# Optimization experiments

Measured on AMD Instinct MI355X. Metric: run time of the kernel, lower is better.

The kernel has to match this reference:

```python
import jax, jax.numpy as jnp
import numpy as np
from jax import lax

STRIDE = 1
PAD = 1


def conv2d(x, w, b, stride=STRIDE, pad=PAD):
    out = lax.conv_general_dilated(x, w, (stride, stride), [(pad, pad), (pad, pad)],
                                   dimension_numbers=('NCHW', 'OIHW', 'NCHW'))
    return out + b[None, :, None, None]


def bilinear_gather(x, py, px):
    # x: [B,C,H,W]; py,px: [B,K,Ho,Wo] float sample coords. Zero outside.
    B, C, H, W = x.shape
    y0 = jnp.floor(py)
    x0 = jnp.floor(px)
    wy = (py - y0)[:, None]  # [B,1,K,Ho,Wo]
    wx = (px - x0)[:, None]
    y0i = y0.astype(jnp.int32)
    x0i = x0.astype(jnp.int32)
    xf = x.reshape(B, C, H * W)

    def gather(yi, xi):
        valid = ((yi >= 0) & (yi < H) & (xi >= 0) & (xi < W))
        yc = jnp.clip(yi, 0, H - 1)
        xc = jnp.clip(xi, 0, W - 1)
        idx = (yc * W + xc).reshape(B, 1, -1)
        v = jnp.take_along_axis(xf, idx, axis=2).reshape(B, C, *yi.shape[1:])
        return v * valid[:, None].astype(x.dtype)

    v00 = gather(y0i, x0i)
    v01 = gather(y0i, x0i + 1)
    v10 = gather(y0i + 1, x0i)
    v11 = gather(y0i + 1, x0i + 1)
    return (v00 * (1 - wy) * (1 - wx) + v01 * (1 - wy) * wx
            + v10 * wy * (1 - wx) + v11 * wy * wx)  # [B,C,K,Ho,Wo]


def deform_conv2d(x, offset, weight, bias, mask_mod, stride=STRIDE, pad=PAD):
    # torchvision.ops.deform_conv2d semantics, groups=1, dilation=1.
    B, C, H, W = x.shape
    Co, Ci, Kh, Kw = weight.shape
    K = Kh * Kw
    Ho, Wo = offset.shape[2], offset.shape[3]
    off = offset.reshape(B, K, 2, Ho, Wo)
    dy, dx = off[:, :, 0], off[:, :, 1]
    ky, kx = jnp.meshgrid(jnp.arange(Kh), jnp.arange(Kw), indexing='ij')
    base_y = (jnp.arange(Ho) * stride - pad).astype(x.dtype)
    base_x = (jnp.arange(Wo) * stride - pad).astype(x.dtype)
    py = dy + ky.reshape(K)[None, :, None, None] + base_y[None, None, :, None]
    px = dx + kx.reshape(K)[None, :, None, None] + base_x[None, None, None, :]
    vals = bilinear_gather(x, py, px)  # [B,C,K,Ho,Wo]
    if mask_mod is not None:
        vals = vals * mask_mod[:, None]  # modulation mask [B,K,Ho,Wo]
    out = jnp.einsum('bckhw,ock->bohw', vals, weight.reshape(Co, Ci, K))
    if bias is not None:
        out = out + bias[None, :, None, None]
    return out


def setup_inputs() -> dict:
    key = jax.random.key(0)
    ks = jax.random.split(key, 8)
    B, Cin, Cout, H, W, Kh, Kw = 4, 64, 64, 128, 128, 3, 3
    K = Kh * Kw
    n = Cin * Kh * Kw
    stdv = 1.0 / np.sqrt(n)
    inp = jax.random.normal(ks[0], (B, Cin, H, W), dtype=jnp.float32)
    mask_in = (jax.random.uniform(ks[1], (B, 1, H, W)) > 0.25).astype(jnp.float32)
    weight = jax.random.uniform(ks[2], (Cout, Cin, Kh, Kw), minval=-stdv, maxval=stdv, dtype=jnp.float32)
    bias = jnp.zeros((Cout,), jnp.float32)
    offset_w = jax.random.normal(ks[3], (2 * K, Cin + 1, Kh, Kw), dtype=jnp.float32) * 0.01
    offset_b = jnp.zeros((2 * K,), jnp.float32)
    mask_w = jax.random.normal(ks[4], (K, Cin + 1, Kh, Kw), dtype=jnp.float32) * 0.01
    mask_b = jnp.zeros((K,), jnp.float32)
    return {'input': inp, 'mask_in': mask_in, 'weight': weight, 'bias': bias,
            'offset_w': offset_w, 'offset_b': offset_b, 'mask_w': mask_w, 'mask_b': mask_b}


def reference(input, mask_in, weight, bias, offset_w, offset_b, mask_w, mask_b):
    xm = jnp.concatenate([input, mask_in], axis=1)
    offset = conv2d(xm, offset_w, offset_b)
    C = input.shape[1]
    Kh, Kw = weight.shape[2], weight.shape[3]
    slide_winsize = float(C * Kh * Kw)  # 1*C*Kh*Kw (maskUpdater out-channels = 1)
    # Partial-conv mask propagation (torch.no_grad in original)
    mask_rep = jnp.broadcast_to(mask_in, input.shape)
    ones_w = jnp.ones((1, C, Kh, Kw), input.dtype)
    um = lax.stop_gradient(deform_conv2d(mask_rep, offset, ones_w, None, None))  # [B,1,Ho,Wo]
    update_mask = jnp.clip(um, 0.0, 1.0)
    dcn_mask = jax.nn.sigmoid(conv2d(xm, mask_w, mask_b))
    raw_out = deform_conv2d(input, offset, weight, bias, dcn_mask)
    output = raw_out * update_mask
    return output, update_mask
```

## Files before the change

### kernel.cpp

```cpp
#include <hip/hip_runtime.h>

#define HH 128
#define WW 128
#define HWSZ (HH*WW)
#define NB 4
#define KK 9
#define PS (HWSZ*8)
#define IMS (12*PS)

typedef _Float16 half8 __attribute__((ext_vector_type(8)));
typedef _Float16 h2    __attribute__((ext_vector_type(2)));
typedef float f32x4    __attribute__((ext_vector_type(4)));

union U4 { uint4 v; unsigned a[4]; };
union HU { unsigned u; h2 h; };

__device__ __forceinline__ short f2h(float f) {
    union { _Float16 h; short s; } u; u.h = (_Float16)f; return u.s;
}
__device__ __forceinline__ void gl_lds16(const short* g, short* l) {
    __builtin_amdgcn_global_load_lds(
        (const __attribute__((address_space(1))) void*)g,
        (__attribute__((address_space(3))) void*)l, 16, 0, 0);
}
__device__ __forceinline__ void gl_lds4(const float* g, float* l) {
    __builtin_amdgcn_global_load_lds(
        (const __attribute__((address_space(1))) void*)g,
        (__attribute__((address_space(3))) void*)l, 4, 0, 0);
}

__global__ __launch_bounds__(256) void prep_kernel(
    const float* __restrict__ input,
    const float* __restrict__ mask_in,
    const float* __restrict__ weight,
    const float* __restrict__ offset_w,
    const float* __restrict__ mask_w,
    short* __restrict__ xt2,
    short* __restrict__ wd2,
    short* __restrict__ wc2)
{
    __shared__ short lds[64 * 104];
    int bid = blockIdx.x;
    if (bid < 1024) {
        int wg = ((bid & 7) << 7) | (bid >> 3);
        int g0 = wg * 64;
        int b  = g0 >> 14;
        int p0 = g0 & (HWSZ - 1);
        int px = threadIdx.x & 63;
        int cq = threadIdx.x >> 6;
#pragma unroll
        for (int it = 0; it < 24; ++it) {
            int c = it * 4 + cq;
            float v;
            if (c < 64)       v = input[((size_t)(b * 64 + c)) * HWSZ + p0 + px];
            else if (c == 64) v = mask_in[(size_t)b * HWSZ + p0 + px];
            else              v = 0.f;
            lds[px * 104 + c] = f2h(v);
        }
        __syncthreads();
#pragma unroll
        for (int it = 0; it < 3; ++it) {
            int idx = it * 256 + threadIdx.x;
            if (idx < 768) {
                int ppx = idx / 12, cb = idx - ppx * 12;
                uint4 v = *(const uint4*)&lds[ppx * 104 + cb * 8];
                *(uint4*)&xt2[(size_t)b * IMS + (size_t)cb * PS + (size_t)(p0 + ppx) * 8] = v;
            }
        }
    } else {
        int idx = (bid - 1024) * 256 + threadIdx.x;
        if (idx < 36864) {
            int j = idx & 7, l = (idx >> 3) & 63, f = idx >> 9;
            int nt = f & 3, t9 = f >> 2;
            int k = t9 % 9, ks = t9 / 9;
            int o = nt * 16 + (l & 15);
            int c = ks * 32 + ((l >> 4) & 3) * 8 + j;
            wd2[idx] = f2h(weight[(o * 64 + c) * 9 + k]);
        }
        if (idx < 27648) {
            int j = idx & 7, l = (idx >> 3) & 63, f = idx >> 9;
            int nt = f & 1, t9 = f >> 1;
            int k = t9 % 9, ks = t9 / 9;
            int o = nt * 16 + (l & 15);
            int c = ks * 32 + ((l >> 4) & 3) * 8 + j;
            float v = 0.f;
            if (c <= 64) {
                if (o < 18)      v = offset_w[(o * 65 + c) * 9 + k];
                else if (o < 27) v = mask_w[((o - 18) * 65 + c) * 9 + k];
            }
            wc2[idx] = f2h(v);
        }
    }
}

__global__ __launch_bounds__(256, 3) void fused_conv_deform(
    const short* __restrict__ xt2, const float* __restrict__ mask_in,
    const half8* __restrict__ wc, const half8* __restrict__ wd,
    const float* __restrict__ offset_b, const float* __restrict__ mask_b,
    const float* __restrict__ bias,
    float* __restrict__ out, float* __restrict__ upd)
{
    __shared__ short xsm[8 * 5 * 68 * 8];
    __shared__ float msm[5 * 68];
    __shared__ float offsm[64 * 28];

    int bid = blockIdx.x;
    int wg = ((bid & 7) << 7) | (bid >> 3);
    int wid = threadIdx.x >> 6, lane = threadIdx.x & 63;
    int r = lane & 15, lg = lane >> 4;
    int gblk = wg * 64;
    int b = gblk >> 14;
    int pblk = gblk & (HWSZ - 1);
    int ib = pblk >> 7, j0b = pblk & 127;
    int g0 = gblk + wid * 16;
    int gp = g0 + r;
    int p = gp & (HWSZ - 1);
    int i = p >> 7, j = p & 127;
    const short* xq = xt2 + (size_t)b * IMS + (size_t)lg * PS;
    const float* mb = mask_in + (size_t)b * HWSZ;

    {
        const short* xg = xt2 + (size_t)b * IMS;
#pragma unroll
        for (int it = 0; it < 11; ++it) {
            int idx = it * 256 + threadIdx.x;
            if (idx < 2720) {
                int rb = idx / 68, tc = idx - rb * 68;
                int cb = rb / 5,  tr = rb - cb * 5;
                int row_g = min(max(ib - 2 + tr, 0), HH - 1);
                int col_g = min(max(j0b - 2 + tc, 0), WW - 1);
                gl_lds16(&xg[(size_t)cb * PS + (size_t)(row_g * WW + col_g) * 8],
                         &xsm[idx * 8]);
            }
        }
#pragma unroll
        for (int it = 0; it < 2; ++it) {
            int idx = it * 256 + threadIdx.x;
            if (idx < 340) {
                int tr = idx / 68, tc = idx - tr * 68;
                int row_g = min(max(ib - 2 + tr, 0), HH - 1);
                int col_g = min(max(j0b - 2 + tc, 0), WW - 1);
                gl_lds4(&mb[row_g * WW + col_g], &msm[idx]);
            }
        }
    }

    {
        f32x4 ca0 = {0,0,0,0}, ca1 = {0,0,0,0};
#pragma unroll
        for (int t = 0; t < 9; ++t) {
            int yy = i + t / 3 - 1, xx = j + t % 3 - 1;
            bool v = ((unsigned)yy < HH) && ((unsigned)xx < WW);
            int nb = (v ? yy * WW + xx : 0) * 8;
            union { half8 s8; uint4 u; } A[3];
#pragma unroll
            for (int ks = 0; ks < 3; ++ks) {
                A[ks].u = *(const uint4*)(xq + (size_t)ks * 4 * PS + nb);
                if (!v) { A[ks].u.x = 0; A[ks].u.y = 0; A[ks].u.z = 0; A[ks].u.w = 0; }
            }
#pragma unroll
            for (int ks = 0; ks < 3; ++ks) {
                const half8* wck = wc + ((ks * 9 + t) * 2) * 64 + lane;
                half8 B0 = wck[0];
                half8 B1 = wck[64];
                ca0 = __builtin_amdgcn_mfma_f32_16x16x32_f16(A[ks].s8, B0, ca0, 0, 0, 0);
                ca1 = __builtin_amdgcn_mfma_f32_16x16x32_f16(A[ks].s8, B1, ca1, 0, 0, 0);
            }
        }
        int oc = lane & 15, pr0 = lg * 4;
#pragma unroll
        for (int rr = 0; rr < 4; ++rr) {
            int pxl = wid * 16 + pr0 + rr;
            offsm[pxl * 28 + oc] = ca0[rr] + offset_b[oc];
            int oc2 = 16 + oc;
            if (oc2 < 18) {
                offsm[pxl * 28 + oc2] = ca1[rr] + offset_b[oc2];
            } else if (oc2 < 27) {
                float z = ca1[rr] + mask_b[oc2 - 18];
                offsm[pxl * 28 + oc2] = 1.f / (1.f + __expf(-z));
            }
        }
    }
    asm volatile("s_waitcnt vmcnt(0)" ::: "memory");
    __syncthreads();

    float ov[28];
    {
        int pxl = wid * 16 + r;
#pragma unroll
        for (int q = 0; q < 7; ++q) {
            float4 t = *(const float4*)&offsm[pxl * 28 + q * 4];
            ov[4*q+0] = t.x; ov[4*q+1] = t.y; ov[4*q+2] = t.z; ov[4*q+3] = t.w;
        }
    }

    f32x4 acc0 = {0,0,0,0}, acc1 = {0,0,0,0}, acc2 = {0,0,0,0}, acc3 = {0,0,0,0};
    float um = 0.f;

#pragma unroll
    for (int k = 0; k < KK; ++k) {
        float dy = ov[2*k], dx = ov[2*k+1], m = ov[18+k];
        float py  = dy + (float)(k / 3 + i - 1);
        float pxx = dx + (float)(k % 3 + j - 1);
        float fy = floorf(py), fx = floorf(pxx);
        float wy = py - fy, wx = pxx - fx;
        int y0 = (int)fy, x0 = (int)fx;
        int y1 = y0 + 1, x1 = x0 + 1;
        bool vy0 = (unsigned)y0 < HH, vy1 = (unsigned)y1 < HH;
        bool vx0 = (unsigned)x0 < WW, vx1 = (unsigned)x1 < WW;
        int yc0 = min(max(y0, 0), HH - 1), yc1 = min(max(y1, 0), HH - 1);
        int xc0 = min(max(x0, 0), WW - 1), xc1 = min(max(x1, 0), WW - 1);
        float r00 = (vy0 && vx0) ? (1.f - wy) * (1.f - wx) : 0.f;
        float r01 = (vy0 && vx1) ? (1.f - wy) * wx : 0.f;
        float r10 = (vy1 && vx0) ? wy * (1.f - wx) : 0.f;
        float r11 = (vy1 && vx1) ? wy * wx : 0.f;

        int tr0 = yc0 - ib + 2, tr1 = yc1 - ib + 2;
        int tc0 = xc0 - j0b + 2, tc1 = xc1 - j0b + 2;
        bool in00 = ((unsigned)tr0 < 5u) & ((unsigned)tc0 < 68u);
        bool in01 = ((unsigned)tr0 < 5u) & ((unsigned)tc1 < 68u);
        bool in10 = ((unsigned)tr1 < 5u) & ((unsigned)tc0 < 68u);
        bool in11 = ((unsigned)tr1 < 5u) & ((unsigned)tc1 < 68u);
        int trc0 = min(max(tr0, 0), 4), trc1 = min(max(tr1, 0), 4);
        int tcc0 = min(max(tc0, 0), 67), tcc1 = min(max(tc1, 0), 67);
        int l00 = (trc0 * 68 + tcc0), l01 = (trc0 * 68 + tcc1);
        int l10 = (trc1 * 68 + tcc0), l11 = (trc1 * 68 + tcc1);

        U4 g00[2], g01[2], g10[2], g11[2];
#pragma unroll
        for (int ks = 0; ks < 2; ++ks) {
            const short* xs = xsm + (size_t)(ks * 4 + lg) * (5 * 68 * 8);
            g00[ks].v = *(const uint4*)(xs + l00 * 8);
            g01[ks].v = *(const uint4*)(xs + l01 * 8);
            g10[ks].v = *(const uint4*)(xs + l10 * 8);
            g11[ks].v = *(const uint4*)(xs + l11 * 8);
        }
        float m00 = msm[l00], m01 = msm[l01], m10 = msm[l10], m11 = msm[l11];

        if (!__all(in00 & in01 & in10 & in11)) {
            int p00 = yc0 * WW + xc0, p01 = yc0 * WW + xc1;
            int p10 = yc1 * WW + xc0, p11 = yc1 * WW + xc1;
            if (!in00) {
                g00[0].v = *(const uint4*)(xq + (size_t)p00 * 8);
                g00[1].v = *(const uint4*)(xq + 4 * PS + (size_t)p00 * 8);
                m00 = mb[p00];
            }
            if (!in01) {
                g01[0].v = *(const uint4*)(xq + (size_t)p01 * 8);
                g01[1].v = *(const uint4*)(xq + 4 * PS + (size_t)p01 * 8);
                m01 = mb[p01];
            }
            if (!in10) {
                g10[0].v = *(const uint4*)(xq + (size_t)p10 * 8);
                g10[1].v = *(const uint4*)(xq + 4 * PS + (size_t)p10 * 8);
                m10 = mb[p10];
            }
            if (!in11) {
                g11[0].v = *(const uint4*)(xq + (size_t)p11 * 8);
                g11[1].v = *(const uint4*)(xq + 4 * PS + (size_t)p11 * 8);
                m11 = mb[p11];
            }
        }

        um += r00 * m00 + r01 * m01 + r10 * m10 + r11 * m11;

        float w00 = r00 * m, w01 = r01 * m, w10 = r10 * m, w11 = r11 * m;
        h2 w00h = { (_Float16)w00, (_Float16)w00 };
        h2 w01h = { (_Float16)w01, (_Float16)w01 };
        h2 w10h = { (_Float16)w10, (_Float16)w10 };
        h2 w11h = { (_Float16)w11, (_Float16)w11 };

#pragma unroll
        for (int ks = 0; ks < 2; ++ks) {
            union { half8 s8; unsigned u[4]; } A;
#pragma unroll
            for (int q = 0; q < 4; ++q) {
                HU a00, a01, a10, a11, res;
                a00.u = g00[ks].a[q]; a01.u = g01[ks].a[q];
                a10.u = g10[ks].a[q]; a11.u = g11[ks].a[q];
                h2 acc = a00.h * w00h;
                acc = a01.h * w01h + acc;
                acc = a10.h * w10h + acc;
                acc = a11.h * w11h + acc;
                res.h = acc;
                A.u[q] = res.u;
            }
            const half8* wbk = wd + ((ks * 9 + k) * 4) * 64 + lane;
            half8 B0 = wbk[0];
            half8 B1 = wbk[64];
            half8 B2 = wbk[128];
            half8 B3 = wbk[192];
            acc0 = __builtin_amdgcn_mfma_f32_16x16x32_f16(A.s8, B0, acc0, 0, 0, 0);
            acc1 = __builtin_amdgcn_mfma_f32_16x16x32_f16(A.s8, B1, acc1, 0, 0, 0);
            acc2 = __builtin_amdgcn_mfma_f32_16x16x32_f16(A.s8, B2, acc2, 0, 0, 0);
            acc3 = __builtin_amdgcn_mfma_f32_16x16x32_f16(A.s8, B3, acc3, 0, 0, 0);
        }
    }

    um = fminf(fmaxf(64.f * um, 0.f), 1.f);
    if (lane < 16) upd[g0 + lane] = um;

    int oc = lane & 15;
    int pr0 = lg * 4;
    float u[4];
#pragma unroll
    for (int rr = 0; rr < 4; ++rr) u[rr] = __shfl(um, pr0 + rr, 64);

    __syncthreads();
    float* outsm = (float*)xsm;
#define STORE_NT(ACC, NT)                                                     \
    {                                                                         \
        float bo = bias[(NT) * 16 + oc];                                      \
        _Pragma("unroll")                                                     \
        for (int rr = 0; rr < 4; ++rr) {                                      \
            int pxl = wid * 16 + pr0 + rr;                                    \
            outsm[pxl * 65 + (NT) * 16 + oc] = (ACC[rr] + bo) * u[rr];        \
        }                                                                     \
    }
    STORE_NT(acc0, 0)
    STORE_NT(acc1, 1)
    STORE_NT(acc2, 2)
    STORE_NT(acc3, 3)
#undef STORE_NT
    __syncthreads();
    {
        int ch = threadIdx.x >> 2, q = threadIdx.x & 3;
        float tmp[16];
#pragma unroll
        for (int mI = 0; mI < 16; ++mI)
            tmp[mI] = outsm[(q * 16 + mI) * 65 + ch];
        float4* dst = (float4*)(out + ((size_t)(b * 64 + ch)) * HWSZ + pblk + q * 16);
#pragma unroll
        for (int gq = 0; gq < 4; ++gq) {
            float4 v = { tmp[4*gq], tmp[4*gq+1], tmp[4*gq+2], tmp[4*gq+3] };
            dst[gq] = v;
        }
    }
}

extern "C" void kernel_launch(void* const* d_in, const int* in_sizes, int n_in,
                              void* d_out, int out_size, void* d_ws, size_t ws_size,
                              hipStream_t stream) {
    const float* input    = (const float*)d_in[0];
    const float* mask_in  = (const float*)d_in[1];
    const float* weight   = (const float*)d_in[2];
    const float* bias     = (const float*)d_in[3];
    const float* offset_w = (const float*)d_in[4];
    const float* offset_b = (const float*)d_in[5];
    const float* mask_w   = (const float*)d_in[6];
    const float* mask_b   = (const float*)d_in[7];

    float* out = (float*)d_out;
    float* upd = out + (size_t)NB * 64 * HWSZ;

    short* wd2 = (short*)d_ws;
    short* wc2 = wd2 + 36864;
    short* xt2 = wc2 + 27648;

    hipLaunchKernelGGL(prep_kernel, dim3(1168), dim3(256), 0, stream,
                       input, mask_in, weight, offset_w, mask_w, xt2, wd2, wc2);
    hipLaunchKernelGGL(fused_conv_deform, dim3(1024), dim3(256), 0, stream,
                       xt2, mask_in, (const half8*)wc2, (const half8*)wd2,
                       offset_b, mask_b, bias, out, upd);
}
```

Measured before the change: 43.17 us.

## Process two output rows per block and feed offset conv from the LDS tile

Each workgroup now covers a 2x64 pixel tile instead of 64 pixels, staging a 6-row halo tile in LDS. The offset/mask conv reads its A operands from that LDS tile (and folds the mask channel in via msm) rather than from global memory. Weight fragments are loaded once and reused across both rows. Offsets are stored as fp16 in LDS. The grid halves and launch bounds drop to 2 blocks per CU, which raises per-thread register use and lowers occupancy; the fp16 offsets reduce precision of the sampling coordinates.

```diff
diff --git a/kernel.cpp b/kernel.cpp
--- a/kernel.cpp
+++ b/kernel.cpp
@@ -7,6 +7,9 @@
 #define KK 9
 #define PS (HWSZ*8)
 #define IMS (12*PS)
+#define TROWS 6
+#define TCOLS 68
+#define TPX (TROWS*TCOLS)
 
 typedef _Float16 half8 __attribute__((ext_vector_type(8)));
 typedef _Float16 h2    __attribute__((ext_vector_type(2)));
@@ -93,247 +96,318 @@
     }
 }
 
-__global__ __launch_bounds__(256, 3) void fused_conv_deform(
+__global__ __launch_bounds__(256, 2) void fused_conv_deform(
     const short* __restrict__ xt2, const float* __restrict__ mask_in,
     const half8* __restrict__ wc, const half8* __restrict__ wd,
     const float* __restrict__ offset_b, const float* __restrict__ mask_b,
     const float* __restrict__ bias,
     float* __restrict__ out, float* __restrict__ upd)
 {
-    __shared__ short xsm[8 * 5 * 68 * 8];
-    __shared__ float msm[5 * 68];
-    __shared__ float offsm[64 * 28];
+    __shared__ short xsm[8 * TPX * 8];
+    __shared__ float msm[TPX];
+    __shared__ short offsm[128 * 32];
 
     int bid = blockIdx.x;
-    int wg = ((bid & 7) << 7) | (bid >> 3);
-    int wid = threadIdx.x >> 6, lane = threadIdx.x & 63;
+    int wg = ((bid & 7) << 6) | (bid >> 3);
+    int w = threadIdx.x >> 6, lane = threadIdx.x & 63;
     int r = lane & 15, lg = lane >> 4;
-    int gblk = wg * 64;
-    int b = gblk >> 14;
-    int pblk = gblk & (HWSZ - 1);
-    int ib = pblk >> 7, j0b = pblk & 127;
-    int g0 = gblk + wid * 16;
-    int gp = g0 + r;
-    int p = gp & (HWSZ - 1);
-    int i = p >> 7, j = p & 127;
-    const short* xq = xt2 + (size_t)b * IMS + (size_t)lg * PS;
+    int b = wg >> 7;
+    int rem = wg & 127;
+    int ib = (rem >> 1) * 2;
+    int j0b = (rem & 1) * 64;
+    int jw = j0b + w * 16;
+    int jj0 = jw + r;
+
+    const short* xg = xt2 + (size_t)b * IMS;
+    const short* xq = xg + (size_t)lg * PS;
     const float* mb = mask_in + (size_t)b * HWSZ;
 
-    {
-        const short* xg = xt2 + (size_t)b * IMS;
-#pragma unroll
-        for (int it = 0; it < 11; ++it) {
-            int idx = it * 256 + threadIdx.x;
-            if (idx < 2720) {
-                int rb = idx / 68, tc = idx - rb * 68;
-                int cb = rb / 5,  tr = rb - cb * 5;
-                int row_g = min(max(ib - 2 + tr, 0), HH - 1);
-                int col_g = min(max(j0b - 2 + tc, 0), WW - 1);
-                gl_lds16(&xg[(size_t)cb * PS + (size_t)(row_g * WW + col_g) * 8],
-                         &xsm[idx * 8]);
-            }
-        }
+#pragma unroll
+    for (int cb = 0; cb < 8; ++cb) {
 #pragma unroll
         for (int it = 0; it < 2; ++it) {
             int idx = it * 256 + threadIdx.x;
-            if (idx < 340) {
-                int tr = idx / 68, tc = idx - tr * 68;
-                int row_g = min(max(ib - 2 + tr, 0), HH - 1);
-                int col_g = min(max(j0b - 2 + tc, 0), WW - 1);
-                gl_lds4(&mb[row_g * WW + col_g], &msm[idx]);
-            }
-        }
-    }
-
-    {
-        f32x4 ca0 = {0,0,0,0}, ca1 = {0,0,0,0};
-#pragma unroll
-        for (int t = 0; t < 9; ++t) {
-            int yy = i + t / 3 - 1, xx = j + t % 3 - 1;
-            bool v = ((unsigned)yy < HH) && ((unsigned)xx < WW);
-            int nb = (v ? yy * WW + xx : 0) * 8;
-            union { half8 s8; uint4 u; } A[3];
-#pragma unroll
-            for (int ks = 0; ks < 3; ++ks) {
-                A[ks].u = *(const uint4*)(xq + (size_t)ks * 4 * PS + nb);
-                if (!v) { A[ks].u.x = 0; A[ks].u.y = 0; A[ks].u.z = 0; A[ks].u.w = 0; }
-            }
-#pragma unroll
-            for (int ks = 0; ks < 3; ++ks) {
-                const half8* wck = wc + ((ks * 9 + t) * 2) * 64 + lane;
-                half8 B0 = wck[0];
-                half8 B1 = wck[64];
-                ca0 = __builtin_amdgcn_mfma_f32_16x16x32_f16(A[ks].s8, B0, ca0, 0, 0, 0);
-                ca1 = __builtin_amdgcn_mfma_f32_16x16x32_f16(A[ks].s8, B1, ca1, 0, 0, 0);
-            }
-        }
-        int oc = lane & 15, pr0 = lg * 4;
-#pragma unroll
-        for (int rr = 0; rr < 4; ++rr) {
-            int pxl = wid * 16 + pr0 + rr;
-            offsm[pxl * 28 + oc] = ca0[rr] + offset_b[oc];
-            int oc2 = 16 + oc;
-            if (oc2 < 18) {
-                offsm[pxl * 28 + oc2] = ca1[rr] + offset_b[oc2];
-            } else if (oc2 < 27) {
-                float z = ca1[rr] + mask_b[oc2 - 18];
-                offsm[pxl * 28 + oc2] = 1.f / (1.f + __expf(-z));
-            }
+            if (idx < TPX) {
+                int tr = idx / TCOLS, tc = idx - tr * TCOLS;
+                int rg = min(max(ib - 2 + tr, 0), HH - 1);
+                int cg = min(max(j0b - 2 + tc, 0), WW - 1);
+                gl_lds16(&xg[(size_t)cb * PS + (size_t)(rg * WW + cg) * 8],
+                         &xsm[(cb * TPX + idx) * 8]);
+            }
+        }
+    }
+#pragma unroll
+    for (int it = 0; it < 2; ++it) {
+        int idx = it * 256 + threadIdx.x;
+        if (idx < TPX) {
+            int tr = idx / TCOLS, tc = idx - tr * TCOLS;
+            int rg = min(max(ib - 2 + tr, 0), HH - 1);
+            int cg = min(max(j0b - 2 + tc, 0), WW - 1);
+            gl_lds4(&mb[rg * WW + cg], &msm[idx]);
         }
     }
     asm volatile("s_waitcnt vmcnt(0)" ::: "memory");
     __syncthreads();
 
-    float ov[28];
     {
-        int pxl = wid * 16 + r;
-#pragma unroll
-        for (int q = 0; q < 7; ++q) {
-            float4 t = *(const float4*)&offsm[pxl * 28 + q * 4];
-            ov[4*q+0] = t.x; ov[4*q+1] = t.y; ov[4*q+2] = t.z; ov[4*q+3] = t.w;
-        }
-    }
-
-    f32x4 acc0 = {0,0,0,0}, acc1 = {0,0,0,0}, acc2 = {0,0,0,0}, acc3 = {0,0,0,0};
-    float um = 0.f;
+        f32x4 ca00 = {0,0,0,0}, ca01 = {0,0,0,0};
+        f32x4 ca10 = {0,0,0,0}, ca11 = {0,0,0,0};
+#pragma unroll
+        for (int t = 0; t < 9; ++t) {
+            int dr = t / 3 - 1, dc = t % 3 - 1;
+            const half8* wck = wc + (t * 2) * 64 + lane;
+            half8 Bk0n0 = wck[0],        Bk0n1 = wck[64];
+            half8 Bk1n0 = wck[9*2*64],   Bk1n1 = wck[9*2*64 + 64];
+            half8 Bk2n0 = wck[18*2*64],  Bk2n1 = wck[18*2*64 + 64];
+#pragma unroll
+            for (int s = 0; s < 2; ++s) {
+                int ii = ib + s + dr, jj = jj0 + dc;
+                bool valid = ((unsigned)ii < HH) && ((unsigned)jj < WW);
+                int tr = ii - (ib - 2), tc = jj - (j0b - 2);
+                int loff = (tr * TCOLS + tc) * 8;
+                union { half8 s8; uint4 u; } A0, A1, A2;
+                A0.u = *(const uint4*)&xsm[lg * (TPX * 8) + loff];
+                A1.u = *(const uint4*)&xsm[(4 + lg) * (TPX * 8) + loff];
+                if (!valid) {
+                    A0.u.x = 0; A0.u.y = 0; A0.u.z = 0; A0.u.w = 0;
+                    A1.u.x = 0; A1.u.y = 0; A1.u.z = 0; A1.u.w = 0;
+                }
+                unsigned am = (valid && lg == 0)
+                            ? (unsigned)(unsigned short)f2h(msm[tr * TCOLS + tc]) : 0u;
+                A2.u.x = am; A2.u.y = 0; A2.u.z = 0; A2.u.w = 0;
+                if (s == 0) {
+                    ca00 = __builtin_amdgcn_mfma_f32_16x16x32_f16(A0.s8, Bk0n0, ca00, 0, 0, 0);
+                    ca01 = __builtin_amdgcn_mfma_f32_16x16x32_f16(A0.s8, Bk0n1, ca01, 0, 0, 0);
+                    ca00 = __builtin_amdgcn_mfma_f32_16x16x32_f16(A1.s8, Bk1n0, ca00, 0, 0, 0);
+                    ca01 = __builtin_amdgcn_mfma_f32_16x16x32_f16(A1.s8, Bk1n1, ca01, 0, 0, 0);
+                    ca00 = __builtin_amdgcn_mfma_f32_16x16x32_f16(A2.s8, Bk2n0, ca00, 0, 0, 0);
+                    ca01 = __builtin_amdgcn_mfma_f32_16x16x32_f16(A2.s8, Bk2n1, ca01, 0, 0, 0);
+                } else {
+                    ca10 = __builtin_amdgcn_mfma_f32_16x16x32_f16(A0.s8, Bk0n0, ca10, 0, 0, 0);
+                    ca11 = __builtin_amdgcn_mfma_f32_16x16x32_f16(A0.s8, Bk0n1, ca11, 0, 0, 0);
+                    ca10 = __builtin_amdgcn_mfma_f32_16x16x32_f16(A1.s8, Bk1n0, ca10, 0, 0, 0);
+                    ca11 = __builtin_amdgcn_mfma_f32_16x16x32_f16(A1.s8, Bk1n1, ca11, 0, 0, 0);
+                    ca10 = __builtin_amdgcn_mfma_f32_16x16x32_f16(A2.s8, Bk2n0, ca10, 0, 0, 0);
+                    ca11 = __builtin_amdgcn_mfma_f32_16x16x32_f16(A2.s8, Bk2n1, ca11, 0, 0, 0);
+                }
+            }
+        }
+        int oc = lane & 15, pr0 = lg * 4;
+#pragma unroll
+        for (int s = 0; s < 2; ++s) {
+            const f32x4& c0 = s ? ca10 : ca00;
+            const f32x4& c1 = s ? ca11 : ca01;
+#pragma unroll
+            for (int rr = 0; rr < 4; ++rr) {
+                int px = s * 64 + w * 16 + pr0 + rr;
+                offsm[px * 32 + oc] = f2h(c0[rr] + offset_b[oc]);
+                int oc2 = 16 + oc;
+                if (oc2 < 18) {
+                    offsm[px * 32 + oc2] = f2h(c1[rr] + offset_b[oc2]);
+                } else if (oc2 < 27) {
+                    float z = c1[rr] + mask_b[oc2 - 18];
+                    offsm[px * 32 + oc2] = f2h(1.f / (1.f + __expf(-z)));
+                }
+            }
+        }
+    }
+    __syncthreads();
+
+    float ov0[28], ov1[28];
+#pragma unroll
+    for (int s = 0; s < 2; ++s) {
+        int px = s * 64 + w * 16 + r;
+        float* ov = s ? ov1 : ov0;
+        const U4* op = (const U4*)&offsm[px * 32];
+#pragma unroll
+        for (int q4 = 0; q4 < 4; ++q4) {
+            U4 t = op[q4];
+#pragma unroll
+            for (int e = 0; e < 4; ++e) {
+                int base = q4 * 8 + e * 2;
+                if (base < 28) {
+                    HU hu; hu.u = t.a[e];
+                    ov[base] = (float)hu.h[0];
+                    ov[base + 1] = (float)hu.h[1];
+                }
+            }
+        }
+    }
+
+    f32x4 ac00 = {0,0,0,0}, ac01 = {0,0,0,0}, ac02 = {0,0,0,0}, ac03 = {0,0,0,0};
+    f32x4 ac10 = {0,0,0,0}, ac11 = {0,0,0,0}, ac12 = {0,0,0,0}, ac13 = {0,0,0,0};
+    float um0 = 0.f, um1 = 0.f;
 
 #pragma unroll
     for (int k = 0; k < KK; ++k) {
-        float dy = ov[2*k], dx = ov[2*k+1], m = ov[18+k];
-        float py  = dy + (float)(k / 3 + i - 1);
-        float pxx = dx + (float)(k % 3 + j - 1);
-        float fy = floorf(py), fx = floorf(pxx);
-        float wy = py - fy, wx = pxx - fx;
-        int y0 = (int)fy, x0 = (int)fx;
-        int y1 = y0 + 1, x1 = x0 + 1;
-        bool vy0 = (unsigned)y0 < HH, vy1 = (unsigned)y1 < HH;
-        bool vx0 = (unsigned)x0 < WW, vx1 = (unsigned)x1 < WW;
-        int yc0 = min(max(y0, 0), HH - 1), yc1 = min(max(y1, 0), HH - 1);
-        int xc0 = min(max(x0, 0), WW - 1), xc1 = min(max(x1, 0), WW - 1);
-        float r00 = (vy0 && vx0) ? (1.f - wy) * (1.f - wx) : 0.f;
-        float r01 = (vy0 && vx1) ? (1.f - wy) * wx : 0.f;
-        float r10 = (vy1 && vx0) ? wy * (1.f - wx) : 0.f;
-        float r11 = (vy1 && vx1) ? wy * wx : 0.f;
-
-        int tr0 = yc0 - ib + 2, tr1 = yc1 - ib + 2;
-        int tc0 = xc0 - j0b + 2, tc1 = xc1 - j0b + 2;
-        bool in00 = ((unsigned)tr0 < 5u) & ((unsigned)tc0 < 68u);
-        bool in01 = ((unsigned)tr0 < 5u) & ((unsigned)tc1 < 68u);
-        bool in10 = ((unsigned)tr1 < 5u) & ((unsigned)tc0 < 68u);
-        bool in11 = ((unsigned)tr1 < 5u) & ((unsigned)tc1 < 68u);
-        int trc0 = min(max(tr0, 0), 4), trc1 = min(max(tr1, 0), 4);
-        int tcc0 = min(max(tc0, 0), 67), tcc1 = min(max(tc1, 0), 67);
-        int l00 = (trc0 * 68 + tcc0), l01 = (trc0 * 68 + tcc1);
-        int l10 = (trc1 * 68 + tcc0), l11 = (trc1 * 68 + tcc1);
-
-        U4 g00[2], g01[2], g10[2], g11[2];
-#pragma unroll
-        for (int ks = 0; ks < 2; ++ks) {
-            const short* xs = xsm + (size_t)(ks * 4 + lg) * (5 * 68 * 8);
-            g00[ks].v = *(const uint4*)(xs + l00 * 8);
-            g01[ks].v = *(const uint4*)(xs + l01 * 8);
-            g10[ks].v = *(const uint4*)(xs + l10 * 8);
-            g11[ks].v = *(const uint4*)(xs + l11 * 8);
-        }
-        float m00 = msm[l00], m01 = msm[l01], m10 = msm[l10], m11 = msm[l11];
-
-        if (!__all(in00 & in01 & in10 & in11)) {
-            int p00 = yc0 * WW + xc0, p01 = yc0 * WW + xc1;
-            int p10 = yc1 * WW + xc0, p11 = yc1 * WW + xc1;
-            if (!in00) {
-                g00[0].v = *(const uint4*)(xq + (size_t)p00 * 8);
-                g00[1].v = *(const uint4*)(xq + 4 * PS + (size_t)p00 * 8);
-                m00 = mb[p00];
-            }
-            if (!in01) {
-                g01[0].v = *(const uint4*)(xq + (size_t)p01 * 8);
-                g01[1].v = *(const uint4*)(xq + 4 * PS + (size_t)p01 * 8);
-                m01 = mb[p01];
-            }
-            if (!in10) {
-                g10[0].v = *(const uint4*)(xq + (size_t)p10 * 8);
-                g10[1].v = *(const uint4*)(xq + 4 * PS + (size_t)p10 * 8);
-                m10 = mb[p10];
-            }
-            if (!in11) {
-                g11[0].v = *(const uint4*)(xq + (size_t)p11 * 8);
-                g11[1].v = *(const uint4*)(xq + 4 * PS + (size_t)p11 * 8);
-                m11 = mb[p11];
-            }
-        }
-
-        um += r00 * m00 + r01 * m01 + r10 * m10 + r11 * m11;
-
-        float w00 = r00 * m, w01 = r01 * m, w10 = r10 * m, w11 = r11 * m;
-        h2 w00h = { (_Float16)w00, (_Float16)w00 };
-        h2 w01h = { (_Float16)w01, (_Float16)w01 };
-        h2 w10h = { (_Float16)w10, (_Float16)w10 };
-        h2 w11h = { (_Float16)w11, (_Float16)w11 };
-
-#pragma unroll
-        for (int ks = 0; ks < 2; ++ks) {
-            union { half8 s8; unsigned u[4]; } A;
-#pragma unroll
-            for (int q = 0; q < 4; ++q) {
-                HU a00, a01, a10, a11, res;
-                a00.u = g00[ks].a[q]; a01.u = g01[ks].a[q];
-                a10.u = g10[ks].a[q]; a11.u = g11[ks].a[q];
-                h2 acc = a00.h * w00h;
-                acc = a01.h * w01h + acc;
-                acc = a10.h * w10h + acc;
-                acc = a11.h * w11h + acc;
-                res.h = acc;
-                A.u[q] = res.u;
-            }
-            const half8* wbk = wd + ((ks * 9 + k) * 4) * 64 + lane;
-            half8 B0 = wbk[0];
-            half8 B1 = wbk[64];
-            half8 B2 = wbk[128];
-            half8 B3 = wbk[192];
-            acc0 = __builtin_amdgcn_mfma_f32_16x16x32_f16(A.s8, B0, acc0, 0, 0, 0);
-            acc1 = __builtin_amdgcn_mfma_f32_16x16x32_f16(A.s8, B1, acc1, 0, 0, 0);
-            acc2 = __builtin_amdgcn_mfma_f32_16x16x32_f16(A.s8, B2, acc2, 0, 0, 0);
-            acc3 = __builtin_amdgcn_mfma_f32_16x16x32_f16(A.s8, B3, acc3, 0, 0, 0);
-        }
-    }
-
-    um = fminf(fmaxf(64.f * um, 0.f), 1.f);
-    if (lane < 16) upd[g0 + lane] = um;
+        const half8* w0 = wd + ((0 * 9 + k) * 4) * 64 + lane;
+        const half8* w1 = wd + ((1 * 9 + k) * 4) * 64 + lane;
+        half8 B00 = w0[0], B01 = w0[64], B02 = w0[128], B03 = w0[192];
+        half8 B10 = w1[0], B11 = w1[64], B12 = w1[128], B13 = w1[192];
+
+#pragma unroll
+        for (int s = 0; s < 2; ++s) {
+            const float* ov = s ? ov1 : ov0;
+            int i = ib + s, j = jj0;
+            float dy = ov[2*k], dx = ov[2*k+1], m = ov[18+k];
+            float py  = dy + (float)(k / 3 + i - 1);
+            float pxx = dx + (float)(k % 3 + j - 1);
+            float fy = floorf(py), fx = floorf(pxx);
+            float wy = py - fy, wx = pxx - fx;
+            int y0 = (int)fy, x0 = (int)fx;
+            int y1 = y0 + 1, x1 = x0 + 1;
+            bool vy0 = (unsigned)y0 < HH, vy1 = (unsigned)y1 < HH;
+            bool vx0 = (unsigned)x0 < WW, vx1 = (unsigned)x1 < WW;
+            int yc0 = min(max(y0, 0), HH - 1), yc1 = min(max(y1, 0), HH - 1);
+            int xc0 = min(max(x0, 0), WW - 1), xc1 = min(max(x1, 0), WW - 1);
+            float r00 = (vy0 && vx0) ? (1.f - wy) * (1.f - wx) : 0.f;
+            float r01 = (vy0 && vx1) ? (1.f - wy) * wx : 0.f;
+            float r10 = (vy1 && vx0) ? wy * (1.f - wx) : 0.f;
+            float r11 = (vy1 && vx1) ? wy * wx : 0.f;
+
+            int tr0 = yc0 - (ib - 2), tr1 = yc1 - (ib - 2);
+            int tc0 = xc0 - (j0b - 2), tc1 = xc1 - (j0b - 2);
+            bool in00 = ((unsigned)tr0 < (unsigned)TROWS) & ((unsigned)tc0 < (unsigned)TCOLS);
+            bool in01 = ((unsigned)tr0 < (unsigned)TROWS) & ((unsigned)tc1 < (unsigned)TCOLS);
+            bool in10 = ((unsigned)tr1 < (unsigned)TROWS) & ((unsigned)tc0 < (unsigned)TCOLS);
+            bool in11 = ((unsigned)tr1 < (unsigned)TROWS) & ((unsigned)tc1 < (unsigned)TCOLS);
+            int trc0 = min(max(tr0, 0), TROWS - 1), trc1 = min(max(tr1, 0), TROWS - 1);
+            int tcc0 = min(max(tc0, 0), TCOLS - 1), tcc1 = min(max(tc1, 0), TCOLS - 1);
+            int l00 = trc0 * TCOLS + tcc0, l01 = trc0 * TCOLS + tcc1;
+            int l10 = trc1 * TCOLS + tcc0, l11 = trc1 * TCOLS + tcc1;
+
+            U4 g00[2], g01[2], g10[2], g11[2];
+#pragma unroll
+            for (int ks = 0; ks < 2; ++ks) {
+                const short* xs = xsm + (size_t)(ks * 4 + lg) * (TPX * 8);
+                g00[ks].v = *(const uint4*)(xs + l00 * 8);
+                g01[ks].v = *(const uint4*)(xs + l01 * 8);
+                g10[ks].v = *(const uint4*)(xs + l10 * 8);
+                g11[ks].v = *(const uint4*)(xs + l11 * 8);
+            }
+            float m00 = msm[l00], m01 = msm[l01], m10 = msm[l10], m11 = msm[l11];
+
+            if (!__all(in00 & in01 & in10 & in11)) {
+                int p00 = yc0 * WW + xc0, p01 = yc0 * WW + xc1;
+                int p10 = yc1 * WW + xc0, p11 = yc1 * WW + xc1;
+                if (!in00) {
+                    g00[0].v = *(const uint4*)(xq + (size_t)p00 * 8);
+                    g00[1].v = *(const uint4*)(xq + 4 * PS + (size_t)p00 * 8);
+                    m00 = mb[p00];
+                }
+                if (!in01) {
+                    g01[0].v = *(const uint4*)(xq + (size_t)p01 * 8);
+                    g01[1].v = *(const uint4*)(xq + 4 * PS + (size_t)p01 * 8);
+                    m01 = mb[p01];
+                }
+                if (!in10) {
+                    g10[0].v = *(const uint4*)(xq + (size_t)p10 * 8);
+                    g10[1].v = *(const uint4*)(xq + 4 * PS + (size_t)p10 * 8);
+                    m10 = mb[p10];
+                }
+                if (!in11) {
+                    g11[0].v = *(const uint4*)(xq + (size_t)p11 * 8);
+                    g11[1].v = *(const uint4*)(xq + 4 * PS + (size_t)p11 * 8);
+                    m11 = mb[p11];
+                }
+            }
+
+            float umv = r00 * m00 + r01 * m01 + r10 * m10 + r11 * m11;
+            if (s == 0) um0 += umv; else um1 += umv;
+
+            float w00 = r00 * m, w01 = r01 * m, w10 = r10 * m, w11 = r11 * m;
+            h2 w00h = { (_Float16)w00, (_Float16)w00 };
+            h2 w01h = { (_Float16)w01, (_Float16)w01 };
+            h2 w10h = { (_Float16)w10, (_Float16)w10 };
+            h2 w11h = { (_Float16)w11, (_Float16)w11 };
+
+#pragma unroll
+            for (int ks = 0; ks < 2; ++ks) {
+                union { half8 s8; unsigned u[4]; } A;
+#pragma unroll
+                for (int q = 0; q < 4; ++q) {
+                    HU a00, a01, a10, a11, res;
+                    a00.u = g00[ks].a[q]; a01.u = g01[ks].a[q];
+                    a10.u = g10[ks].a[q]; a11.u = g11[ks].a[q];
+                    h2 acc = a00.h * w00h;
+                    acc = a01.h * w01h + acc;
+                    acc = a10.h * w10h + acc;
+                    acc = a11.h * w11h + acc;
+                    res.h = acc;
+                    A.u[q] = res.u;
+                }
+                if (s == 0) {
+                    if (ks == 0) {
+                        ac00 = __builtin_amdgcn_mfma_f32_16x16x32_f16(A.s8, B00, ac00, 0, 0, 0);
+                        ac01 = __builtin_amdgcn_mfma_f32_16x16x32_f16(A.s8, B01, ac01, 0, 0, 0);
+                        ac02 = __builtin_amdgcn_mfma_f32_16x16x32_f16(A.s8, B02, ac02, 0, 0, 0);
+                        ac03 = __builtin_amdgcn_mfma_f32_16x16x32_f16(A.s8, B03, ac03, 0, 0, 0);
+                    } else {
+                        ac00 = __builtin_amdgcn_mfma_f32_16x16x32_f16(A.s8, B10, ac00, 0, 0, 0);
+                        ac01 = __builtin_amdgcn_mfma_f32_16x16x32_f16(A.s8, B11, ac01, 0, 0, 0);
+                        ac02 = __builtin_amdgcn_mfma_f32_16x16x32_f16(A.s8, B12, ac02, 0, 0, 0);
+                        ac03 = __builtin_amdgcn_mfma_f32_16x16x32_f16(A.s8, B13, ac03, 0, 0, 0);
+                    }
+                } else {
+                    if (ks == 0) {
+                        ac10 = __builtin_amdgcn_mfma_f32_16x16x32_f16(A.s8, B00, ac10, 0, 0, 0);
+                        ac11 = __builtin_amdgcn_mfma_f32_16x16x32_f16(A.s8, B01, ac11, 0, 0, 0);
+                        ac12 = __builtin_amdgcn_mfma_f32_16x16x32_f16(A.s8, B02, ac12, 0, 0, 0);
+                        ac13 = __builtin_amdgcn_mfma_f32_16x16x32_f16(A.s8, B03, ac13, 0, 0, 0);
+                    } else {
+                        ac10 = __builtin_amdgcn_mfma_f32_16x16x32_f16(A.s8, B10, ac10, 0, 0, 0);
+                        ac11 = __builtin_amdgcn_mfma_f32_16x16x32_f16(A.s8, B11, ac11, 0, 0, 0);
+                        ac12 = __builtin_amdgcn_mfma_f32_16x16x32_f16(A.s8, B12, ac12, 0, 0, 0);
+                        ac13 = __builtin_amdgcn_mfma_f32_16x16x32_f16(A.s8, B13, ac13, 0, 0, 0);
+                    }
+                }
+            }
+        }
+    }
+
+    um0 = fminf(fmaxf(64.f * um0, 0.f), 1.f);
+    um1 = fminf(fmaxf(64.f * um1, 0.f), 1.f);
+    if (lane < 16) {
+        upd[(size_t)b * HWSZ + (ib + 0) * WW + jw + lane] = um0;
+        upd[(size_t)b * HWSZ + (ib + 1) * WW + jw + lane] = um1;
+    }
 
     int oc = lane & 15;
     int pr0 = lg * 4;
-    float u[4];
-#pragma unroll
-    for (int rr = 0; rr < 4; ++rr) u[rr] = __shfl(um, pr0 + rr, 64);
+    float u0[4], u1[4];
+#pragma unroll
+    for (int rr = 0; rr < 4; ++rr) {
+        u0[rr] = __shfl(um0, pr0 + rr, 64);
+        u1[rr] = __shfl(um1, pr0 + rr, 64);
+    }
 
     __syncthreads();
     float* outsm = (float*)xsm;
-#define STORE_NT(ACC, NT)                                                     \
+#define STORE_NT(ACC, NT, S, U)                                               \
     {                                                                         \
         float bo = bias[(NT) * 16 + oc];                                      \
         _Pragma("unroll")                                                     \
         for (int rr = 0; rr < 4; ++rr) {                                      \
-            int pxl = wid * 16 + pr0 + rr;                                    \
-            outsm[pxl * 65 + (NT) * 16 + oc] = (ACC[rr] + bo) * u[rr];        \
+            int px = (S) * 64 + w * 16 + pr0 + rr;                            \
+            outsm[px * 65 + (NT) * 16 + oc] = (ACC[rr] + bo) * U[rr];         \
         }                                                                     \
     }
-    STORE_NT(acc0, 0)
-    STORE_NT(acc1, 1)
-    STORE_NT(acc2, 2)
-    STORE_NT(acc3, 3)
+    STORE_NT(ac00, 0, 0, u0) STORE_NT(ac01, 1, 0, u0)
+    STORE_NT(ac02, 2, 0, u0) STORE_NT(ac03, 3, 0, u0)
+    STORE_NT(ac10, 0, 1, u1) STORE_NT(ac11, 1, 1, u1)
+    STORE_NT(ac12, 2, 1, u1) STORE_NT(ac13, 3, 1, u1)
 #undef STORE_NT
     __syncthreads();
     {
         int ch = threadIdx.x >> 2, q = threadIdx.x & 3;
-        float tmp[16];
-#pragma unroll
-        for (int mI = 0; mI < 16; ++mI)
-            tmp[mI] = outsm[(q * 16 + mI) * 65 + ch];
-        float4* dst = (float4*)(out + ((size_t)(b * 64 + ch)) * HWSZ + pblk + q * 16);
-#pragma unroll
-        for (int gq = 0; gq < 4; ++gq) {
-            float4 v = { tmp[4*gq], tmp[4*gq+1], tmp[4*gq+2], tmp[4*gq+3] };
-            dst[gq] = v;
+        int row = q >> 1, colh = (q & 1) * 32;
+        float* dst = out + ((size_t)(b * 64 + ch)) * HWSZ + (ib + row) * WW + j0b + colh;
+#pragma unroll
+        for (int gq = 0; gq < 8; ++gq) {
+            int px = q * 32 + gq * 4;
+            float4 v = { outsm[(px + 0) * 65 + ch], outsm[(px + 1) * 65 + ch],
+                         outsm[(px + 2) * 65 + ch], outsm[(px + 3) * 65 + ch] };
+            *(float4*)(dst + gq * 4) = v;
         }
     }
 }
@@ -359,7 +433,7 @@
 
     hipLaunchKernelGGL(prep_kernel, dim3(1168), dim3(256), 0, stream,
                        input, mask_in, weight, offset_w, mask_w, xt2, wd2, wc2);
-    hipLaunchKernelGGL(fused_conv_deform, dim3(1024), dim3(256), 0, stream,
+    hipLaunchKernelGGL(fused_conv_deform, dim3(512), dim3(256), 0, stream,
                        xt2, mask_in, (const half8*)wc2, (const half8*)wd2,
                        offset_b, mask_b, bias, out, upd);
 }
```

Measured after the change: 39.74 us (median of 2 runs). -8.0%, faster.
